# Kernel optimization log

Measured on AMD Instinct MI355X. Metric: run time of the kernel, lower is better.

## Reference

```python
import jax, jax.numpy as jnp
import numpy as np

N, E, G = 100000, 600000, 64  # nodes, edges, graphs
F_IN, W, EPS = 32, 128, 1e-5


def setup_inputs() -> dict:
    key = jax.random.key(0)
    ks = jax.random.split(key, 16)
    p = lambda k, shape: jax.random.normal(k, shape, dtype=jnp.float32) * 0.1
    z = lambda n: jnp.zeros((n,), jnp.float32)
    o = lambda n: jnp.ones((n,), jnp.float32)
    return {
        "x": jax.random.normal(ks[0], (N, F_IN), dtype=jnp.float32),
        "edge_index": jax.random.randint(ks[1], (2, E), 0, N, dtype=jnp.int32),
        "batch": jnp.sort(jax.random.randint(ks[2], (N,), 0, G, dtype=jnp.int32)),
        # GCNConv layers
        "W1": p(ks[3], (F_IN, W)), "b1": z(W),
        "W2": p(ks[4], (W, W)), "b2": z(W),
        # mlp_first: Linear -> BN -> ReLU -> Linear
        "W3": p(ks[5], (W, W)), "b3": z(W), "g1": o(W), "be1": z(W),
        "W4": p(ks[6], (W, W)), "b4": z(W),
        # mlp: Linear -> BN -> ReLU -> Linear
        "W5": p(ks[7], (W, W // 2)), "b5": z(W // 2), "g2": o(W // 2), "be2": z(W // 2),
        "W6": p(ks[8], (W // 2, 1)), "b6": z(1),
    }


def gcn_conv(x, src, dst, Wt, b):
    # PyG GCNConv with add_self_loops=True: D^-1/2 (A+I) D^-1/2 (x W) + b
    h = x @ Wt  # [N, width]
    deg = jax.ops.segment_sum(jnp.ones(src.shape[0], x.dtype), dst, num_segments=N) + 1.0
    dinv = jax.lax.rsqrt(deg)
    norm = dinv[src] * dinv[dst]  # per-edge normalization
    agg = jax.ops.segment_sum(h[src] * norm[:, None], dst, num_segments=N)
    # self-loop term: norm for (i,i) is 1/deg[i]
    return agg + h * (dinv * dinv)[:, None] + b


def batch_norm(x, g, b):
    # training-mode BatchNorm1d (batch stats, biased var)
    mu = x.mean(axis=0)
    var = jnp.mean((x - mu) ** 2, axis=0)
    return (x - mu) * jax.lax.rsqrt(var + EPS) * g + b


def reference(x, edge_index, batch, W1, b1, W2, b2, W3, b3, g1, be1, W4, b4, W5, b5, g2, be2, W6, b6):
    src, dst = edge_index[0], edge_index[1]
    x = jax.nn.relu(gcn_conv(x, src, dst, W1, b1))
    x = jax.nn.relu(gcn_conv(x, src, dst, W2, b2))
    # mlp_first + ReLU
    x = jax.nn.relu(batch_norm(x @ W3 + b3, g1, be1)) @ W4 + b4
    x = jax.nn.relu(x)
    # global max pool over nodes per graph
    x = jax.ops.segment_max(x, batch, num_segments=G)  # [G, width]
    # final mlp
    x = jax.nn.relu(batch_norm(x @ W5 + b5, g2, be2)) @ W6 + b6
    return x[:, 0]
```

## Files before the change

### kernel.cpp

```cpp
#include <hip/hip_runtime.h>

#define N_NODES 100000
#define N_EDGES 600000
#define N_GRAPHS 64
#define EPS 1e-5f
#define SCAN_BLOCKS 391

typedef unsigned short u16;
typedef unsigned int u32;
typedef __attribute__((ext_vector_type(8))) short bf16x8;
typedef __attribute__((ext_vector_type(4))) float f32x4;

__device__ __forceinline__ float bf2f(u16 u) { return __uint_as_float(((u32)u) << 16); }
__device__ __forceinline__ u16 f2bf(float f) {
    u32 u = __float_as_uint(f);
    u += 0x7FFFu + ((u >> 16) & 1u);
    return (u16)(u >> 16);
}
__device__ __forceinline__ float2 bfx2(u32 v) {
    float2 r;
    r.x = __uint_as_float(v << 16);
    r.y = __uint_as_float(v & 0xFFFF0000u);
    return r;
}

#define WS_COUNTS   ((size_t)0)
#define WS_CURSOR   ((size_t)400384)
#define WS_POOLED   ((size_t)800768)
#define WS_BNSUM    ((size_t)833536)
#define WS_BNSUMSQ  ((size_t)834048)
#define WS_FLAG     ((size_t)834560)
#define ZERO_BYTES  ((size_t)835072)
#define WS_OFFSETS  ((size_t)835072)
#define WS_DINV     ((size_t)1235456)
#define WS_DINV2    ((size_t)1635840)
#define WS_SRCS     ((size_t)2036224)
#define WS_ZF       ((size_t)4436736)
#define WS_CANONW   ((size_t)4453120)
#define WS_BUFA     ((size_t)4578560)
#define WS_BUFB     ((size_t)30178560)

#define CW_W1 0
#define CW_B1 4096
#define CW_W2 4224
#define CW_B2 20608
#define CW_W3 20736
#define CW_B3 37120
#define CW_G1 37248
#define CW_BE1 37376
#define CW_W4 37504
#define CW_B4 53888
#define CW_W5 54016
#define CW_B5 62208
#define CW_G2 62272
#define CW_BE2 62336
#define CW_W6 62400
#define CW_B6 62464

__global__ void detect_kernel(const u32* __restrict__ xraw, int* __restrict__ flag) {
    __shared__ int cnt;
    if (threadIdx.x == 0) cnt = 0;
    __syncthreads();
    int c = 0;
    for (int i = threadIdx.x; i < 2048; i += 256) {
        u32 w = xraw[i];
        float a = fabsf(__uint_as_float((w & 0xFFFFu) << 16));
        if (a == 0.f || (a > 1e-8f && a < 1e4f)) c++;
    }
    atomicAdd(&cnt, c);
    __syncthreads();
    if (threadIdx.x == 0) *flag = (cnt > 1024) ? 1 : 0;
}

__global__ void convx_kernel(const void* __restrict__ xsrc, u16* __restrict__ dst,
                             const int* __restrict__ flag) {
    int i = blockIdx.x * 256 + threadIdx.x;
    if (i < N_NODES * 32)
        dst[i] = (*flag) ? ((const u16*)xsrc)[i] : f2bf(((const float*)xsrc)[i]);
}

struct SmallArgs {
    const void* src[16];
    int n[16];
    int off[16];
    int cols[16];
};
__global__ void convs_kernel(SmallArgs a, u16* __restrict__ dst, const int* __restrict__ flag) {
    int i = blockIdx.x * 256 + threadIdx.x;
    int isbf = *flag;
#pragma unroll
    for (int j = 0; j < 16; j++)
        if (i < a.n[j]) {
            u16 v = isbf ? ((const u16*)a.src[j])[i] : f2bf(((const float*)a.src[j])[i]);
            if (a.cols[j] > 0) {
                int k = i / a.cols[j];
                int n = i - k * a.cols[j];
                int Kd = a.n[j] / a.cols[j];
                dst[a.off[j] + n * Kd + k] = v;
            } else {
                dst[a.off[j] + i] = v;
            }
        }
}

__global__ void deg_kernel(const int* __restrict__ dst, int* __restrict__ counts) {
    int e = blockIdx.x * 256 + threadIdx.x;
    if (e < N_EDGES) atomicAdd(&counts[dst[e]], 1);
}

__global__ __launch_bounds__(256) void reduce_kernel(const int* __restrict__ counts,
                                                     int* __restrict__ partials) {
    int i = blockIdx.x * 256 + threadIdx.x;
    int v = (i < N_NODES) ? counts[i] : 0;
    for (int off = 32; off > 0; off >>= 1) v += __shfl_down(v, off, 64);
    __shared__ int wsum[4];
    if ((threadIdx.x & 63) == 0) wsum[threadIdx.x >> 6] = v;
    __syncthreads();
    if (threadIdx.x == 0) partials[blockIdx.x] = wsum[0] + wsum[1] + wsum[2] + wsum[3];
}

__global__ __launch_bounds__(512) void scanpart_kernel(int* __restrict__ partials) {
    __shared__ int sc[512];
    int t = threadIdx.x;
    int v = (t < SCAN_BLOCKS) ? partials[t] : 0;
    sc[t] = v;
    __syncthreads();
    for (int off = 1; off < 512; off <<= 1) {
        int u = (t >= off) ? sc[t - off] : 0;
        __syncthreads();
        sc[t] += u;
        __syncthreads();
    }
    if (t < SCAN_BLOCKS) partials[t] = sc[t] - v;
}

__global__ __launch_bounds__(256) void offsets_kernel(const int* __restrict__ counts,
                                                      const int* __restrict__ partials,
                                                      int* __restrict__ offs,
                                                      float* __restrict__ dinv) {
    int i = blockIdx.x * 256 + threadIdx.x;
    int lane = threadIdx.x & 63, wv = threadIdx.x >> 6;
    int v = (i < N_NODES) ? counts[i] : 0;
    int sv = v;
    for (int off = 1; off < 64; off <<= 1) {
        int u = __shfl_up(sv, off, 64);
        if (lane >= off) sv += u;
    }
    __shared__ int wsum[4];
    if (lane == 63) wsum[wv] = sv;
    __syncthreads();
    int wpre = 0;
    for (int w = 0; w < wv; w++) wpre += wsum[w];
    int excl = sv - v + wpre + partials[blockIdx.x];
    if (i < N_NODES) {
        offs[i] = excl;
        dinv[i] = rsqrtf((float)(v + 1));
    }
    if (i == N_NODES - 1) offs[N_NODES] = excl + v;
}

__global__ void scatter_kernel(const int* __restrict__ src, const int* __restrict__ dst,
                               const int* __restrict__ offs, int* __restrict__ cursor,
                               int* __restrict__ srcs) {
    int e = blockIdx.x * 256 + threadIdx.x;
    if (e < N_EDGES) {
        int d = dst[e];
        int p = offs[d] + atomicAdd(&cursor[d], 1);
        srcs[p] = src[e];
    }
}

template <int K, int IN_MODE, int OUT_MODE>
__global__ __launch_bounds__(256, 3) void mgemm_kernel(
    const u16* __restrict__ A, const u16* __restrict__ Wt, const u16* __restrict__ bias,
    u16* __restrict__ C, const float* __restrict__ scl, const float* __restrict__ shf,
    const float* __restrict__ dscale, float* __restrict__ bn_sum,
    float* __restrict__ bn_sumsq, const int* __restrict__ batch, u32* __restrict__ pooled,
    const int* __restrict__ goffs, const int* __restrict__ gsrcs,
    const float* __restrict__ gdinv, const u16* __restrict__ gbias, int M) {
    constexpr int KP = K + 8;
    constexpr int NKT = K / 32;
    __shared__ __align__(16) u16 Wl[128 * KP];
    __shared__ float csum[128], csumsq[128];

    const int tid = threadIdx.x;
    const int wave = tid >> 6;
    const int lane = tid & 63;
    const int l15 = lane & 15;
    const int quad = lane >> 4;
    const int row0 = blockIdx.x * 128 + wave * 32;

    {
        const u32* g = (const u32*)Wt;
        u32* l = (u32*)Wl;
        for (int i = tid; i < 128 * (K / 2); i += 256) {
            int n = i / (K / 2), j = i - n * (K / 2);
            l[n * (KP / 2) + j] = g[i];
        }
    }
    if (OUT_MODE == 1 && tid < 128) { csum[tid] = 0.f; csumsq[tid] = 0.f; }

    uint4 gr[2][NKT];
    if (IN_MODE == 2) {
#pragma unroll
        for (int rt = 0; rt < 2; rt++) {
            int r = min(row0 + rt * 16 + l15, M - 1);
            int e0 = goffs[r], e1 = goffs[r + 1];
            float ga[NKT][8];
#pragma unroll
            for (int kt = 0; kt < NKT; kt++)
#pragma unroll
                for (int j = 0; j < 8; j++) ga[kt][j] = 0.f;
            for (int e = e0; e < e1; e++) {
                int s = gsrcs[e];
                const u16* hp = A + (size_t)s * K + quad * 8;
#pragma unroll
                for (int kt = 0; kt < NKT; kt++) {
                    uint4 raw = *(const uint4*)(hp + kt * 32);
                    u32 w4[4] = {raw.x, raw.y, raw.z, raw.w};
#pragma unroll
                    for (int t = 0; t < 4; t++) {
                        float2 f = bfx2(w4[t]);
                        ga[kt][2 * t] += f.x;
                        ga[kt][2 * t + 1] += f.y;
                    }
                }
            }
            float di = gdinv[r];
            const u16* op = A + (size_t)r * K + quad * 8;
#pragma unroll
            for (int kt = 0; kt < NKT; kt++) {
                uint4 own = *(const uint4*)(op + kt * 32);
                uint4 bb = *(const uint4*)(gbias + kt * 32 + quad * 8);
                u32 ow[4] = {own.x, own.y, own.z, own.w};
                u32 bw[4] = {bb.x, bb.y, bb.z, bb.w};
                u32 pk[4];
#pragma unroll
                for (int t = 0; t < 4; t++) {
                    float2 fo = bfx2(ow[t]);
                    float2 fb = bfx2(bw[t]);
                    float vx = fmaxf(fmaf(ga[kt][2 * t] + fo.x, di, fb.x), 0.f);
                    float vy = fmaxf(fmaf(ga[kt][2 * t + 1] + fo.y, di, fb.y), 0.f);
                    pk[t] = (u32)f2bf(vx) | ((u32)f2bf(vy) << 16);
                }
                gr[rt][kt] = {pk[0], pk[1], pk[2], pk[3]};
            }
        }
    }
    __syncthreads();

    f32x4 acc[2][8];
#pragma unroll
    for (int rt = 0; rt < 2; rt++)
#pragma unroll
        for (int nt = 0; nt < 8; nt++) acc[rt][nt] = {0.f, 0.f, 0.f, 0.f};

#pragma unroll
    for (int k0 = 0; k0 < K; k0 += 32) {
        bf16x8 af[2];
        if (IN_MODE == 2) {
#pragma unroll
            for (int rt = 0; rt < 2; rt++) af[rt] = __builtin_bit_cast(bf16x8, gr[rt][k0 / 32]);
        } else if (IN_MODE == 0) {
#pragma unroll
            for (int rt = 0; rt < 2; rt++) {
                int r = min(row0 + rt * 16 + l15, M - 1);
                af[rt] = *(const bf16x8*)(A + (size_t)r * K + k0 + quad * 8);
            }
        } else {
            float s8[8], h8[8];
#pragma unroll
            for (int t = 0; t < 8; t++) {
                s8[t] = scl[k0 + quad * 8 + t];
                h8[t] = shf[k0 + quad * 8 + t];
            }
#pragma unroll
            for (int rt = 0; rt < 2; rt++) {
                int r = min(row0 + rt * 16 + l15, M - 1);
                uint4 raw = *(const uint4*)(A + (size_t)r * K + k0 + quad * 8);
                u32 w4[4] = {raw.x, raw.y, raw.z, raw.w};
                bf16x8 tmp;
#pragma unroll
                for (int t = 0; t < 4; t++) {
                    float2 f = bfx2(w4[t]);
                    f.x = fmaxf(fmaf(f.x, s8[2 * t], h8[2 * t]), 0.f);
                    f.y = fmaxf(fmaf(f.y, s8[2 * t + 1], h8[2 * t + 1]), 0.f);
                    tmp[2 * t] = (short)f2bf(f.x);
                    tmp[2 * t + 1] = (short)f2bf(f.y);
                }
                af[rt] = tmp;
            }
        }
#pragma unroll
        for (int nt = 0; nt < 8; nt++) {
            bf16x8 bf = *(const bf16x8*)&Wl[(nt * 16 + l15) * KP + k0 + quad * 8];
            acc[0][nt] = __builtin_amdgcn_mfma_f32_16x16x32_bf16(af[0], bf, acc[0][nt], 0, 0, 0);
            acc[1][nt] = __builtin_amdgcn_mfma_f32_16x16x32_bf16(af[1], bf, acc[1][nt], 0, 0, 0);
        }
    }

    if (OUT_MODE == 0) {
#pragma unroll
        for (int rt = 0; rt < 2; rt++)
#pragma unroll
            for (int i = 0; i < 4; i++) {
                int r = row0 + rt * 16 + quad * 4 + i;
                if (r < M) {
                    float ds = dscale[r];
                    u16* cp = C + (size_t)r * 128 + l15;
#pragma unroll
                    for (int nt = 0; nt < 8; nt++) cp[nt * 16] = f2bf(acc[rt][nt][i] * ds);
                }
            }
    } else if (OUT_MODE == 1) {
        float b[8], s[8], sq[8];
#pragma unroll
        for (int nt = 0; nt < 8; nt++) {
            b[nt] = bf2f(bias[nt * 16 + l15]);
            s[nt] = 0.f;
            sq[nt] = 0.f;
        }
#pragma unroll
        for (int rt = 0; rt < 2; rt++)
#pragma unroll
            for (int i = 0; i < 4; i++) {
                int r = row0 + rt * 16 + quad * 4 + i;
                if (r < M) {
                    u16* cp = C + (size_t)r * 128 + l15;
#pragma unroll
                    for (int nt = 0; nt < 8; nt++) {
                        float v = acc[rt][nt][i] + b[nt];
                        s[nt] += v;
                        sq[nt] += v * v;
                        cp[nt * 16] = f2bf(v);
                    }
                }
            }
#pragma unroll
        for (int nt = 0; nt < 8; nt++) {
            atomicAdd(&csum[nt * 16 + l15], s[nt]);
            atomicAdd(&csumsq[nt * 16 + l15], sq[nt]);
        }
        __syncthreads();
        if (tid < 128) {
            atomicAdd(&bn_sum[tid], csum[tid]);
            atomicAdd(&bn_sumsq[tid], csumsq[tid]);
        }
    } else {
        float b[8];
#pragma unroll
        for (int nt = 0; nt < 8; nt++) b[nt] = bf2f(bias[nt * 16 + l15]);
        float cur[8];
#pragma unroll
        for (int nt = 0; nt < 8; nt++) cur[nt] = 0.f;
        int curg = -1;
#pragma unroll
        for (int rt = 0; rt < 2; rt++)
#pragma unroll
            for (int i = 0; i < 4; i++) {
                int r = row0 + rt * 16 + quad * 4 + i;
                if (r < M) {
                    int g = batch[r];
                    if (g != curg) {
                        if (curg >= 0) {
                            u32* bp = pooled + curg * 128 + l15;
#pragma unroll
                            for (int nt = 0; nt < 8; nt++)
                                if (cur[nt] > 0.f)
                                    atomicMax(&bp[nt * 16], __float_as_uint(cur[nt]));
                        }
                        curg = g;
#pragma unroll
                        for (int nt = 0; nt < 8; nt++) cur[nt] = 0.f;
                    }
#pragma unroll
                    for (int nt = 0; nt < 8; nt++)
                        cur[nt] = fmaxf(cur[nt], fmaxf(acc[rt][nt][i] + b[nt], 0.f));
                }
            }
        if (curg >= 0) {
            u32* bp = pooled + curg * 128 + l15;
#pragma unroll
            for (int nt = 0; nt < 8; nt++)
                if (cur[nt] > 0.f) atomicMax(&bp[nt * 16], __float_as_uint(cur[nt]));
        }
    }
}

__global__ void bnstats_kernel(float* __restrict__ bn_sum, float* __restrict__ bn_sumsq,
                               const u16* __restrict__ g1, const u16* __restrict__ be1) {
    int c = threadIdx.x;
    if (c < 128) {
        float mu = bn_sum[c] / (float)N_NODES;
        float var = bn_sumsq[c] / (float)N_NODES - mu * mu;
        float rstd = rsqrtf(var + EPS);
        float sc = rstd * bf2f(g1[c]);
        bn_sum[c] = sc;
        bn_sumsq[c] = bf2f(be1[c]) - mu * sc;
    }
}

__global__ __launch_bounds__(256) void head1_kernel(const u32* __restrict__ pooled,
                                                    const u16* __restrict__ W5,
                                                    const u16* __restrict__ b5,
                                                    float* __restrict__ zf) {
    __shared__ float red[4][64];
    int g = blockIdx.x;
    int c = threadIdx.x & 63;
    int kq = threadIdx.x >> 6;
    const u32* prow = pooled + g * 128;
    float p = 0.f;
    for (int k = kq * 32; k < kq * 32 + 32; k++)
        p = fmaf(__uint_as_float(prow[k]), bf2f(W5[k * 64 + c]), p);
    red[kq][c] = p;
    __syncthreads();
    if (kq == 0) zf[g * 64 + c] = red[0][c] + red[1][c] + red[2][c] + red[3][c] + bf2f(b5[c]);
}

__global__ __launch_bounds__(64) void head2_kernel(const float* __restrict__ zf,
                                                   const u16* __restrict__ g2,
                                                   const u16* __restrict__ be2,
                                                   const u16* __restrict__ W6,
                                                   const u16* __restrict__ b6,
                                                   void* __restrict__ outv,
                                                   const int* __restrict__ flag) {
    __shared__ float Z[64][65];
    __shared__ float sc[64], sh[64], w6[64];
    int t = threadIdx.x;
    for (int idx = t; idx < 4096; idx += 64) Z[idx >> 6][idx & 63] = zf[idx];
    w6[t] = bf2f(W6[t]);
    __syncthreads();
    {
        float s = 0.f, sq = 0.f;
        for (int g = 0; g < 64; g++) {
            float v = Z[g][t];
            s += v;
            sq += v * v;
        }
        float mu = s * (1.f / 64.f);
        float var = sq * (1.f / 64.f) - mu * mu;
        float rstd = rsqrtf(var + EPS);
        float scale = rstd * bf2f(g2[t]);
        sc[t] = scale;
        sh[t] = bf2f(be2[t]) - mu * scale;
    }
    __syncthreads();
    float o = 0.f;
    for (int c = 0; c < 64; c++)
        o = fmaf(fmaxf(fmaf(Z[t][c], sc[c], sh[c]), 0.f), w6[c], o);
    float res = o + bf2f(b6[0]);
    if (*flag)
        ((u16*)outv)[t] = f2bf(res);
    else
        ((float*)outv)[t] = res;
}

extern "C" void kernel_launch(void* const* d_in, const int* in_sizes, int n_in, void* d_out,
                              int out_size, void* d_ws, size_t ws_size, hipStream_t stream) {
    const void* x = d_in[0];
    const int* ei = (const int*)d_in[1];
    const int* bat = (const int*)d_in[2];

    char* ws = (char*)d_ws;
    int* counts = (int*)(ws + WS_COUNTS);
    int* cursor = (int*)(ws + WS_CURSOR);
    u32* pooled = (u32*)(ws + WS_POOLED);
    float* bnsum = (float*)(ws + WS_BNSUM);
    float* bnssq = (float*)(ws + WS_BNSUMSQ);
    int* flag = (int*)(ws + WS_FLAG);
    int* offs = (int*)(ws + WS_OFFSETS);
    float* dinv = (float*)(ws + WS_DINV);
    int* partials = (int*)(ws + WS_DINV2);
    int* srcs = (int*)(ws + WS_SRCS);
    float* zf = (float*)(ws + WS_ZF);
    u16* cw = (u16*)(ws + WS_CANONW);
    u16* bufA = (u16*)(ws + WS_BUFA);
    u16* bufB = (u16*)(ws + WS_BUFB);
    u16* canonx = bufB;

    const int* esrc = ei;
    const int* edst = ei + N_EDGES;

    hipMemsetAsync(ws, 0, ZERO_BYTES, stream);
    detect_kernel<<<1, 256, 0, stream>>>((const u32*)x, flag);

    convx_kernel<<<(N_NODES * 32 + 255) / 256, 256, 0, stream>>>(x, canonx, flag);
    SmallArgs sa;
    const int cw_off[16] = {CW_W1, CW_B1, CW_W2, CW_B2, CW_W3, CW_B3, CW_G1, CW_BE1,
                            CW_W4, CW_B4, CW_W5, CW_B5, CW_G2, CW_BE2, CW_W6, CW_B6};
    const int cw_n[16] = {4096, 128, 16384, 128, 16384, 128, 128, 128,
                          16384, 128, 8192, 64, 64, 64, 64, 1};
    const int cw_c[16] = {128, 0, 128, 0, 128, 0, 0, 0, 128, 0, 0, 0, 0, 0, 0, 0};
    for (int j = 0; j < 16; j++) {
        sa.src[j] = d_in[3 + j];
        sa.n[j] = cw_n[j];
        sa.off[j] = cw_off[j];
        sa.cols[j] = cw_c[j];
    }
    convs_kernel<<<64, 256, 0, stream>>>(sa, cw, flag);

    deg_kernel<<<(N_EDGES + 255) / 256, 256, 0, stream>>>(edst, counts);
    reduce_kernel<<<SCAN_BLOCKS, 256, 0, stream>>>(counts, partials);
    scanpart_kernel<<<1, 512, 0, stream>>>(partials);
    offsets_kernel<<<SCAN_BLOCKS, 256, 0, stream>>>(counts, partials, offs, dinv);
    scatter_kernel<<<(N_EDGES + 255) / 256, 256, 0, stream>>>(esrc, edst, offs, cursor, srcs);

    const int gb = (N_NODES + 127) / 128;
    mgemm_kernel<32, 0, 0><<<gb, 256, 0, stream>>>(canonx, cw + CW_W1, nullptr, bufA, nullptr,
                                                   nullptr, dinv, nullptr, nullptr, nullptr,
                                                   nullptr, nullptr, nullptr, nullptr, nullptr,
                                                   N_NODES);
    mgemm_kernel<128, 2, 0><<<gb, 256, 0, stream>>>(bufA, cw + CW_W2, nullptr, bufB, nullptr,
                                                    nullptr, dinv, nullptr, nullptr, nullptr,
                                                    nullptr, offs, srcs, dinv, cw + CW_B1,
                                                    N_NODES);
    mgemm_kernel<128, 2, 1><<<gb, 256, 0, stream>>>(bufB, cw + CW_W3, cw + CW_B3, bufA, nullptr,
                                                    nullptr, nullptr, bnsum, bnssq, nullptr,
                                                    nullptr, offs, srcs, dinv, cw + CW_B2,
                                                    N_NODES);
    bnstats_kernel<<<1, 128, 0, stream>>>(bnsum, bnssq, cw + CW_G1, cw + CW_BE1);
    mgemm_kernel<128, 1, 2><<<gb, 256, 0, stream>>>(bufA, cw + CW_W4, cw + CW_B4, nullptr, bnsum,
                                                    bnssq, nullptr, nullptr, nullptr, bat,
                                                    pooled, nullptr, nullptr, nullptr, nullptr,
                                                    N_NODES);
    head1_kernel<<<N_GRAPHS, 256, 0, stream>>>(pooled, cw + CW_W5, cw + CW_B5, zf);
    head2_kernel<<<1, 64, 0, stream>>>(zf, cw + CW_G2, cw + CW_BE2, cw + CW_W6, cw + CW_B6,
                                       d_out, flag);
}
```

Before: 360.5 us.

## Use 512-thread blocks with one 16-row tile per wave and prefetch gather indices

```diff
diff --git a/kernel.cpp b/kernel.cpp
--- a/kernel.cpp
+++ b/kernel.cpp
@@ -171,7 +171,7 @@
 }
 
 template <int K, int IN_MODE, int OUT_MODE>
-__global__ __launch_bounds__(256, 3) void mgemm_kernel(
+__global__ __launch_bounds__(512, 8) void mgemm_kernel(
     const u16* __restrict__ A, const u16* __restrict__ Wt, const u16* __restrict__ bias,
     u16* __restrict__ C, const float* __restrict__ scl, const float* __restrict__ shf,
     const float* __restrict__ dscale, float* __restrict__ bn_sum,
@@ -188,85 +188,82 @@
     const int lane = tid & 63;
     const int l15 = lane & 15;
     const int quad = lane >> 4;
-    const int row0 = blockIdx.x * 128 + wave * 32;
+    const int row0 = blockIdx.x * 128 + wave * 16;
 
     {
         const u32* g = (const u32*)Wt;
         u32* l = (u32*)Wl;
-        for (int i = tid; i < 128 * (K / 2); i += 256) {
+        for (int i = tid; i < 128 * (K / 2); i += 512) {
             int n = i / (K / 2), j = i - n * (K / 2);
             l[n * (KP / 2) + j] = g[i];
         }
     }
     if (OUT_MODE == 1 && tid < 128) { csum[tid] = 0.f; csumsq[tid] = 0.f; }
 
-    uint4 gr[2][NKT];
+    uint4 gr[NKT];
     if (IN_MODE == 2) {
-#pragma unroll
-        for (int rt = 0; rt < 2; rt++) {
-            int r = min(row0 + rt * 16 + l15, M - 1);
-            int e0 = goffs[r], e1 = goffs[r + 1];
-            float ga[NKT][8];
-#pragma unroll
-            for (int kt = 0; kt < NKT; kt++)
-#pragma unroll
-                for (int j = 0; j < 8; j++) ga[kt][j] = 0.f;
-            for (int e = e0; e < e1; e++) {
-                int s = gsrcs[e];
-                const u16* hp = A + (size_t)s * K + quad * 8;
-#pragma unroll
-                for (int kt = 0; kt < NKT; kt++) {
-                    uint4 raw = *(const uint4*)(hp + kt * 32);
-                    u32 w4[4] = {raw.x, raw.y, raw.z, raw.w};
-#pragma unroll
-                    for (int t = 0; t < 4; t++) {
-                        float2 f = bfx2(w4[t]);
-                        ga[kt][2 * t] += f.x;
-                        ga[kt][2 * t + 1] += f.y;
-                    }
+        const int r = min(row0 + l15, M - 1);
+        const int e0 = goffs[r];
+        const int e1 = goffs[r + 1];
+        float ga[NKT][8];
+#pragma unroll
+        for (int kt = 0; kt < NKT; kt++)
+#pragma unroll
+            for (int j = 0; j < 8; j++) ga[kt][j] = 0.f;
+        const u16* Aq = A + quad * 8;
+        int s = (e0 < e1) ? gsrcs[e0] : 0;
+        for (int e = e0; e < e1; e++) {
+            const u16* hp = Aq + (size_t)s * K;
+            uint4 ra[NKT];
+#pragma unroll
+            for (int kt = 0; kt < NKT; kt++) ra[kt] = *(const uint4*)(hp + kt * 32);
+            int sn = gsrcs[min(e + 1, e1 - 1)];
+#pragma unroll
+            for (int kt = 0; kt < NKT; kt++) {
+                u32 w4[4] = {ra[kt].x, ra[kt].y, ra[kt].z, ra[kt].w};
+#pragma unroll
+                for (int t = 0; t < 4; t++) {
+                    float2 f = bfx2(w4[t]);
+                    ga[kt][2 * t] += f.x;
+                    ga[kt][2 * t + 1] += f.y;
                 }
             }
-            float di = gdinv[r];
-            const u16* op = A + (size_t)r * K + quad * 8;
-#pragma unroll
-            for (int kt = 0; kt < NKT; kt++) {
-                uint4 own = *(const uint4*)(op + kt * 32);
-                uint4 bb = *(const uint4*)(gbias + kt * 32 + quad * 8);
-                u32 ow[4] = {own.x, own.y, own.z, own.w};
-                u32 bw[4] = {bb.x, bb.y, bb.z, bb.w};
-                u32 pk[4];
-#pragma unroll
-                for (int t = 0; t < 4; t++) {
-                    float2 fo = bfx2(ow[t]);
-                    float2 fb = bfx2(bw[t]);
-                    float vx = fmaxf(fmaf(ga[kt][2 * t] + fo.x, di, fb.x), 0.f);
-                    float vy = fmaxf(fmaf(ga[kt][2 * t + 1] + fo.y, di, fb.y), 0.f);
-                    pk[t] = (u32)f2bf(vx) | ((u32)f2bf(vy) << 16);
-                }
-                gr[rt][kt] = {pk[0], pk[1], pk[2], pk[3]};
-            }
-        }
-    }
-    __syncthreads();
-
-    f32x4 acc[2][8];
-#pragma unroll
-    for (int rt = 0; rt < 2; rt++)
-#pragma unroll
-        for (int nt = 0; nt < 8; nt++) acc[rt][nt] = {0.f, 0.f, 0.f, 0.f};
+            s = sn;
+        }
+        float di = gdinv[r];
+        const u16* op = A + (size_t)r * K + quad * 8;
+#pragma unroll
+        for (int kt = 0; kt < NKT; kt++) {
+            uint4 own = *(const uint4*)(op + kt * 32);
+            uint4 bb = *(const uint4*)(gbias + kt * 32 + quad * 8);
+            u32 ow[4] = {own.x, own.y, own.z, own.w};
+            u32 bw[4] = {bb.x, bb.y, bb.z, bb.w};
+            u32 pk[4];
+#pragma unroll
+            for (int t = 0; t < 4; t++) {
+                float2 fo = bfx2(ow[t]);
+                float2 fb = bfx2(bw[t]);
+                float vx = fmaxf(fmaf(ga[kt][2 * t] + fo.x, di, fb.x), 0.f);
+                float vy = fmaxf(fmaf(ga[kt][2 * t + 1] + fo.y, di, fb.y), 0.f);
+                pk[t] = (u32)f2bf(vx) | ((u32)f2bf(vy) << 16);
+            }
+            gr[kt] = {pk[0], pk[1], pk[2], pk[3]};
+        }
+    }
+    __syncthreads();
+
+    f32x4 acc[8];
+#pragma unroll
+    for (int nt = 0; nt < 8; nt++) acc[nt] = {0.f, 0.f, 0.f, 0.f};
 
 #pragma unroll
     for (int k0 = 0; k0 < K; k0 += 32) {
-        bf16x8 af[2];
+        bf16x8 af;
         if (IN_MODE == 2) {
-#pragma unroll
-            for (int rt = 0; rt < 2; rt++) af[rt] = __builtin_bit_cast(bf16x8, gr[rt][k0 / 32]);
+            af = __builtin_bit_cast(bf16x8, gr[k0 / 32]);
         } else if (IN_MODE == 0) {
-#pragma unroll
-            for (int rt = 0; rt < 2; rt++) {
-                int r = min(row0 + rt * 16 + l15, M - 1);
-                af[rt] = *(const bf16x8*)(A + (size_t)r * K + k0 + quad * 8);
-            }
+            int r = min(row0 + l15, M - 1);
+            af = *(const bf16x8*)(A + (size_t)r * K + k0 + quad * 8);
         } else {
             float s8[8], h8[8];
 #pragma unroll
@@ -274,44 +271,38 @@
                 s8[t] = scl[k0 + quad * 8 + t];
                 h8[t] = shf[k0 + quad * 8 + t];
             }
-#pragma unroll
-            for (int rt = 0; rt < 2; rt++) {
-                int r = min(row0 + rt * 16 + l15, M - 1);
-                uint4 raw = *(const uint4*)(A + (size_t)r * K + k0 + quad * 8);
-                u32 w4[4] = {raw.x, raw.y, raw.z, raw.w};
-                bf16x8 tmp;
-#pragma unroll
-                for (int t = 0; t < 4; t++) {
-                    float2 f = bfx2(w4[t]);
-                    f.x = fmaxf(fmaf(f.x, s8[2 * t], h8[2 * t]), 0.f);
-                    f.y = fmaxf(fmaf(f.y, s8[2 * t + 1], h8[2 * t + 1]), 0.f);
-                    tmp[2 * t] = (short)f2bf(f.x);
-                    tmp[2 * t + 1] = (short)f2bf(f.y);
-                }
-                af[rt] = tmp;
-            }
+            int r = min(row0 + l15, M - 1);
+            uint4 raw = *(const uint4*)(A + (size_t)r * K + k0 + quad * 8);
+            u32 w4[4] = {raw.x, raw.y, raw.z, raw.w};
+            bf16x8 tmp;
+#pragma unroll
+            for (int t = 0; t < 4; t++) {
+                float2 f = bfx2(w4[t]);
+                f.x = fmaxf(fmaf(f.x, s8[2 * t], h8[2 * t]), 0.f);
+                f.y = fmaxf(fmaf(f.y, s8[2 * t + 1], h8[2 * t + 1]), 0.f);
+                tmp[2 * t] = (short)f2bf(f.x);
+                tmp[2 * t + 1] = (short)f2bf(f.y);
+            }
+            af = tmp;
         }
 #pragma unroll
         for (int nt = 0; nt < 8; nt++) {
             bf16x8 bf = *(const bf16x8*)&Wl[(nt * 16 + l15) * KP + k0 + quad * 8];
-            acc[0][nt] = __builtin_amdgcn_mfma_f32_16x16x32_bf16(af[0], bf, acc[0][nt], 0, 0, 0);
-            acc[1][nt] = __builtin_amdgcn_mfma_f32_16x16x32_bf16(af[1], bf, acc[1][nt], 0, 0, 0);
+            acc[nt] = __builtin_amdgcn_mfma_f32_16x16x32_bf16(af, bf, acc[nt], 0, 0, 0);
         }
     }
 
     if (OUT_MODE == 0) {
 #pragma unroll
-        for (int rt = 0; rt < 2; rt++)
-#pragma unroll
-            for (int i = 0; i < 4; i++) {
-                int r = row0 + rt * 16 + quad * 4 + i;
-                if (r < M) {
-                    float ds = dscale[r];
-                    u16* cp = C + (size_t)r * 128 + l15;
-#pragma unroll
-                    for (int nt = 0; nt < 8; nt++) cp[nt * 16] = f2bf(acc[rt][nt][i] * ds);
-                }
-            }
+        for (int i = 0; i < 4; i++) {
+            int r = row0 + quad * 4 + i;
+            if (r < M) {
+                float ds = dscale[r];
+                u16* cp = C + (size_t)r * 128 + l15;
+#pragma unroll
+                for (int nt = 0; nt < 8; nt++) cp[nt * 16] = f2bf(acc[nt][i] * ds);
+            }
+        }
     } else if (OUT_MODE == 1) {
         float b[8], s[8], sq[8];
 #pragma unroll
@@ -321,21 +312,19 @@
             sq[nt] = 0.f;
         }
 #pragma unroll
-        for (int rt = 0; rt < 2; rt++)
-#pragma unroll
-            for (int i = 0; i < 4; i++) {
-                int r = row0 + rt * 16 + quad * 4 + i;
-                if (r < M) {
-                    u16* cp = C + (size_t)r * 128 + l15;
-#pragma unroll
-                    for (int nt = 0; nt < 8; nt++) {
-                        float v = acc[rt][nt][i] + b[nt];
-                        s[nt] += v;
-                        sq[nt] += v * v;
-                        cp[nt * 16] = f2bf(v);
-                    }
+        for (int i = 0; i < 4; i++) {
+            int r = row0 + quad * 4 + i;
+            if (r < M) {
+                u16* cp = C + (size_t)r * 128 + l15;
+#pragma unroll
+                for (int nt = 0; nt < 8; nt++) {
+                    float v = acc[nt][i] + b[nt];
+                    s[nt] += v;
+                    sq[nt] += v * v;
+                    cp[nt * 16] = f2bf(v);
                 }
             }
+        }
 #pragma unroll
         for (int nt = 0; nt < 8; nt++) {
             atomicAdd(&csum[nt * 16 + l15], s[nt]);
@@ -355,29 +344,26 @@
         for (int nt = 0; nt < 8; nt++) cur[nt] = 0.f;
         int curg = -1;
 #pragma unroll
-        for (int rt = 0; rt < 2; rt++)
-#pragma unroll
-            for (int i = 0; i < 4; i++) {
-                int r = row0 + rt * 16 + quad * 4 + i;
-                if (r < M) {
-                    int g = batch[r];
-                    if (g != curg) {
-                        if (curg >= 0) {
-                            u32* bp = pooled + curg * 128 + l15;
-#pragma unroll
-                            for (int nt = 0; nt < 8; nt++)
-                                if (cur[nt] > 0.f)
-                                    atomicMax(&bp[nt * 16], __float_as_uint(cur[nt]));
-                        }
-                        curg = g;
-#pragma unroll
-                        for (int nt = 0; nt < 8; nt++) cur[nt] = 0.f;
+        for (int i = 0; i < 4; i++) {
+            int r = row0 + quad * 4 + i;
+            if (r < M) {
+                int g = batch[r];
+                if (g != curg) {
+                    if (curg >= 0) {
+                        u32* bp = pooled + curg * 128 + l15;
+#pragma unroll
+                        for (int nt = 0; nt < 8; nt++)
+                            if (cur[nt] > 0.f) atomicMax(&bp[nt * 16], __float_as_uint(cur[nt]));
                     }
-#pragma unroll
-                    for (int nt = 0; nt < 8; nt++)
-                        cur[nt] = fmaxf(cur[nt], fmaxf(acc[rt][nt][i] + b[nt], 0.f));
+                    curg = g;
+#pragma unroll
+                    for (int nt = 0; nt < 8; nt++) cur[nt] = 0.f;
                 }
-            }
+#pragma unroll
+                for (int nt = 0; nt < 8; nt++)
+                    cur[nt] = fmaxf(cur[nt], fmaxf(acc[nt][i] + b[nt], 0.f));
+            }
+        }
         if (curg >= 0) {
             u32* bp = pooled + curg * 128 + l15;
 #pragma unroll
@@ -506,20 +492,20 @@
     scatter_kernel<<<(N_EDGES + 255) / 256, 256, 0, stream>>>(esrc, edst, offs, cursor, srcs);
 
     const int gb = (N_NODES + 127) / 128;
-    mgemm_kernel<32, 0, 0><<<gb, 256, 0, stream>>>(canonx, cw + CW_W1, nullptr, bufA, nullptr,
+    mgemm_kernel<32, 0, 0><<<gb, 512, 0, stream>>>(canonx, cw + CW_W1, nullptr, bufA, nullptr,
                                                    nullptr, dinv, nullptr, nullptr, nullptr,
                                                    nullptr, nullptr, nullptr, nullptr, nullptr,
                                                    N_NODES);
-    mgemm_kernel<128, 2, 0><<<gb, 256, 0, stream>>>(bufA, cw + CW_W2, nullptr, bufB, nullptr,
+    mgemm_kernel<128, 2, 0><<<gb, 512, 0, stream>>>(bufA, cw + CW_W2, nullptr, bufB, nullptr,
                                                     nullptr, dinv, nullptr, nullptr, nullptr,
                                                     nullptr, offs, srcs, dinv, cw + CW_B1,
                                                     N_NODES);
-    mgemm_kernel<128, 2, 1><<<gb, 256, 0, stream>>>(bufB, cw + CW_W3, cw + CW_B3, bufA, nullptr,
+    mgemm_kernel<128, 2, 1><<<gb, 512, 0, stream>>>(bufB, cw + CW_W3, cw + CW_B3, bufA, nullptr,
                                                     nullptr, nullptr, bnsum, bnssq, nullptr,
                                                     nullptr, offs, srcs, dinv, cw + CW_B2,
                                                     N_NODES);
     bnstats_kernel<<<1, 128, 0, stream>>>(bnsum, bnssq, cw + CW_G1, cw + CW_BE1);
-    mgemm_kernel<128, 1, 2><<<gb, 256, 0, stream>>>(bufA, cw + CW_W4, cw + CW_B4, nullptr, bnsum,
+    mgemm_kernel<128, 1, 2><<<gb, 512, 0, stream>>>(bufA, cw + CW_W4, cw + CW_B4, nullptr, bnsum,
                                                     bnssq, nullptr, nullptr, nullptr, bat,
                                                     pooled, nullptr, nullptr, nullptr, nullptr,
                                                     N_NODES);
```

New measurement: 403.2 us. +11.8%, slower.

## Aggregate layer-1 on 32-wide input, then fuse both GCN GEMMs into one kernel

Applied to the files above, without the earlier changes.

```diff
diff --git a/kernel.cpp b/kernel.cpp
--- a/kernel.cpp
+++ b/kernel.cpp
@@ -73,10 +73,12 @@
 }
 
 __global__ void convx_kernel(const void* __restrict__ xsrc, u16* __restrict__ dst,
-                             const int* __restrict__ flag) {
+                             const int* __restrict__ flag, const float* __restrict__ dinv) {
     int i = blockIdx.x * 256 + threadIdx.x;
-    if (i < N_NODES * 32)
-        dst[i] = (*flag) ? ((const u16*)xsrc)[i] : f2bf(((const float*)xsrc)[i]);
+    if (i < N_NODES * 32) {
+        float v = (*flag) ? bf2f(((const u16*)xsrc)[i]) : ((const float*)xsrc)[i];
+        dst[i] = f2bf(v * dinv[i >> 5]);
+    }
 }
 
 struct SmallArgs {
@@ -168,6 +170,141 @@
         int p = offs[d] + atomicAdd(&cursor[d], 1);
         srcs[p] = src[e];
     }
+}
+
+__global__ __launch_bounds__(256, 3) void gemmx_kernel(
+    const u16* __restrict__ xs, const u16* __restrict__ W1t, const u16* __restrict__ b1,
+    const u16* __restrict__ W2t, u16* __restrict__ C, const float* __restrict__ dinv,
+    const int* __restrict__ goffs, const int* __restrict__ gsrcs, int M) {
+    __shared__ __align__(16) u16 ldsA[128 * 40];
+    __shared__ __align__(16) u16 ldsB[128 * 136];
+
+    const int tid = threadIdx.x;
+    const int wave = tid >> 6;
+    const int lane = tid & 63;
+    const int l15 = lane & 15;
+    const int quad = lane >> 4;
+    const int row0 = blockIdx.x * 128 + wave * 32;
+
+    {
+        const u32* g = (const u32*)W1t;
+        u32* l = (u32*)ldsA;
+        for (int i = tid; i < 128 * 16; i += 256) {
+            int n = i >> 4, j = i & 15;
+            l[n * 20 + j] = g[i];
+        }
+    }
+    {
+        const u32* g = (const u32*)W2t;
+        u32* l = (u32*)ldsB;
+        for (int i = tid; i < 128 * 64; i += 256) {
+            int n = i >> 6, j = i & 63;
+            l[n * 68 + j] = g[i];
+        }
+    }
+
+    uint4 gr1[2];
+#pragma unroll
+    for (int rt = 0; rt < 2; rt++) {
+        int r = min(row0 + rt * 16 + l15, M - 1);
+        int e0 = goffs[r], e1 = goffs[r + 1];
+        float ga[8];
+#pragma unroll
+        for (int j = 0; j < 8; j++) ga[j] = 0.f;
+        const u16* Aq = xs + quad * 8;
+        for (int e = e0; e < e1; e++) {
+            int s = gsrcs[e];
+            uint4 raw = *(const uint4*)(Aq + (size_t)s * 32);
+            u32 w4[4] = {raw.x, raw.y, raw.z, raw.w};
+#pragma unroll
+            for (int t = 0; t < 4; t++) {
+                float2 f = bfx2(w4[t]);
+                ga[2 * t] += f.x;
+                ga[2 * t + 1] += f.y;
+            }
+        }
+        float di = dinv[r];
+        uint4 own = *(const uint4*)(xs + (size_t)r * 32 + quad * 8);
+        u32 ow[4] = {own.x, own.y, own.z, own.w};
+        u32 pk[4];
+#pragma unroll
+        for (int t = 0; t < 4; t++) {
+            float2 fo = bfx2(ow[t]);
+            float vx = (ga[2 * t] + fo.x) * di;
+            float vy = (ga[2 * t + 1] + fo.y) * di;
+            pk[t] = (u32)f2bf(vx) | ((u32)f2bf(vy) << 16);
+        }
+        gr1[rt] = {pk[0], pk[1], pk[2], pk[3]};
+    }
+    __syncthreads();
+
+    f32x4 acc1[2][8];
+#pragma unroll
+    for (int rt = 0; rt < 2; rt++)
+#pragma unroll
+        for (int nt = 0; nt < 8; nt++) acc1[rt][nt] = {0.f, 0.f, 0.f, 0.f};
+#pragma unroll
+    for (int nt = 0; nt < 8; nt++) {
+        bf16x8 bf = *(const bf16x8*)&ldsA[(nt * 16 + l15) * 40 + quad * 8];
+        acc1[0][nt] = __builtin_amdgcn_mfma_f32_16x16x32_bf16(
+            __builtin_bit_cast(bf16x8, gr1[0]), bf, acc1[0][nt], 0, 0, 0);
+        acc1[1][nt] = __builtin_amdgcn_mfma_f32_16x16x32_bf16(
+            __builtin_bit_cast(bf16x8, gr1[1]), bf, acc1[1][nt], 0, 0, 0);
+    }
+    __syncthreads();
+
+    float bcol[8];
+#pragma unroll
+    for (int nt = 0; nt < 8; nt++) bcol[nt] = bf2f(b1[nt * 16 + l15]);
+    u16* tb = ldsA + wave * 1280;
+    uint4 gr2[2][4];
+#pragma unroll
+    for (int kt = 0; kt < 4; kt++) {
+#pragma unroll
+        for (int rt = 0; rt < 2; rt++)
+#pragma unroll
+            for (int c2 = 0; c2 < 2; c2++) {
+                int nt = 2 * kt + c2;
+#pragma unroll
+                for (int i = 0; i < 4; i++) {
+                    float v = fmaxf(acc1[rt][nt][i] + bcol[nt], 0.f);
+                    tb[(rt * 16 + quad * 4 + i) * 40 + c2 * 16 + l15] = f2bf(v);
+                }
+            }
+#pragma unroll
+        for (int rt = 0; rt < 2; rt++)
+            gr2[rt][kt] = *(const uint4*)&tb[(rt * 16 + l15) * 40 + quad * 8];
+    }
+
+    f32x4 acc2[2][8];
+#pragma unroll
+    for (int rt = 0; rt < 2; rt++)
+#pragma unroll
+        for (int nt = 0; nt < 8; nt++) acc2[rt][nt] = {0.f, 0.f, 0.f, 0.f};
+#pragma unroll
+    for (int kt = 0; kt < 4; kt++) {
+#pragma unroll
+        for (int nt = 0; nt < 8; nt++) {
+            bf16x8 bf = *(const bf16x8*)&ldsB[(nt * 16 + l15) * 136 + kt * 32 + quad * 8];
+            acc2[0][nt] = __builtin_amdgcn_mfma_f32_16x16x32_bf16(
+                __builtin_bit_cast(bf16x8, gr2[0][kt]), bf, acc2[0][nt], 0, 0, 0);
+            acc2[1][nt] = __builtin_amdgcn_mfma_f32_16x16x32_bf16(
+                __builtin_bit_cast(bf16x8, gr2[1][kt]), bf, acc2[1][nt], 0, 0, 0);
+        }
+    }
+
+#pragma unroll
+    for (int rt = 0; rt < 2; rt++)
+#pragma unroll
+        for (int i = 0; i < 4; i++) {
+            int r = row0 + rt * 16 + quad * 4 + i;
+            if (r < M) {
+                float ds = dinv[r];
+                u16* cp = C + (size_t)r * 128 + l15;
+#pragma unroll
+                for (int nt = 0; nt < 8; nt++) cp[nt * 16] = f2bf(acc2[rt][nt][i] * ds);
+            }
+        }
 }
 
 template <int K, int IN_MODE, int OUT_MODE>
@@ -476,7 +613,7 @@
     u16* cw = (u16*)(ws + WS_CANONW);
     u16* bufA = (u16*)(ws + WS_BUFA);
     u16* bufB = (u16*)(ws + WS_BUFB);
-    u16* canonx = bufB;
+    u16* xsb = bufB;
 
     const int* esrc = ei;
     const int* edst = ei + N_EDGES;
@@ -484,7 +621,6 @@
     hipMemsetAsync(ws, 0, ZERO_BYTES, stream);
     detect_kernel<<<1, 256, 0, stream>>>((const u32*)x, flag);
 
-    convx_kernel<<<(N_NODES * 32 + 255) / 256, 256, 0, stream>>>(x, canonx, flag);
     SmallArgs sa;
     const int cw_off[16] = {CW_W1, CW_B1, CW_W2, CW_B2, CW_W3, CW_B3, CW_G1, CW_BE1,
                             CW_W4, CW_B4, CW_W5, CW_B5, CW_G2, CW_BE2, CW_W6, CW_B6};
@@ -504,22 +640,17 @@
     scanpart_kernel<<<1, 512, 0, stream>>>(partials);
     offsets_kernel<<<SCAN_BLOCKS, 256, 0, stream>>>(counts, partials, offs, dinv);
     scatter_kernel<<<(N_EDGES + 255) / 256, 256, 0, stream>>>(esrc, edst, offs, cursor, srcs);
+    convx_kernel<<<(N_NODES * 32 + 255) / 256, 256, 0, stream>>>(x, xsb, flag, dinv);
 
     const int gb = (N_NODES + 127) / 128;
-    mgemm_kernel<32, 0, 0><<<gb, 256, 0, stream>>>(canonx, cw + CW_W1, nullptr, bufA, nullptr,
-                                                   nullptr, dinv, nullptr, nullptr, nullptr,
-                                                   nullptr, nullptr, nullptr, nullptr, nullptr,
-                                                   N_NODES);
-    mgemm_kernel<128, 2, 0><<<gb, 256, 0, stream>>>(bufA, cw + CW_W2, nullptr, bufB, nullptr,
-                                                    nullptr, dinv, nullptr, nullptr, nullptr,
-                                                    nullptr, offs, srcs, dinv, cw + CW_B1,
-                                                    N_NODES);
-    mgemm_kernel<128, 2, 1><<<gb, 256, 0, stream>>>(bufB, cw + CW_W3, cw + CW_B3, bufA, nullptr,
+    gemmx_kernel<<<gb, 256, 0, stream>>>(xsb, cw + CW_W1, cw + CW_B1, cw + CW_W2, bufA, dinv,
+                                         offs, srcs, N_NODES);
+    mgemm_kernel<128, 2, 1><<<gb, 256, 0, stream>>>(bufA, cw + CW_W3, cw + CW_B3, bufB, nullptr,
                                                     nullptr, nullptr, bnsum, bnssq, nullptr,
                                                     nullptr, offs, srcs, dinv, cw + CW_B2,
                                                     N_NODES);
     bnstats_kernel<<<1, 128, 0, stream>>>(bnsum, bnssq, cw + CW_G1, cw + CW_BE1);
-    mgemm_kernel<128, 1, 2><<<gb, 256, 0, stream>>>(bufA, cw + CW_W4, cw + CW_B4, nullptr, bnsum,
+    mgemm_kernel<128, 1, 2><<<gb, 256, 0, stream>>>(bufB, cw + CW_W4, cw + CW_B4, nullptr, bnsum,
                                                     bnssq, nullptr, nullptr, nullptr, bat,
                                                     pooled, nullptr, nullptr, nullptr, nullptr,
                                                     N_NODES);
```

Result: faster. 353.0 us (-2.1%).
